# Kernel tuning notes

Hardware: AMD Instinct MI355X
Metric: run time of the kernel (lower is better)

Reference implementation:

```python
import jax, jax.numpy as jnp
import numpy as np

B, C, H, W = 2048, 6, 128, 96
OUT_H, OUT_W = 32, 24  # PIL resize((24, 32)) -> width=24, height=32

def setup_inputs() -> dict:
    key = jax.random.key(0)
    kx, ky = jax.random.split(key)
    x = jax.random.normal(kx, (B, C, H, W), dtype=jnp.float32)
    y = jax.random.randint(ky, (B,), 0, 10, dtype=jnp.int32)  # unused by forward
    return {"x": x, "y": y}

def reference(x, y):
    # Batched bilinear resize of every (batch, channel) image from (H, W) to (32, 24).
    # antialias=True matches PIL's BILINEAR triangle filter with scaled support
    # when downsampling. Batch/channel dims keep their size -> identity along them.
    resized = jax.image.resize(
        x, (x.shape[0], x.shape[1], OUT_H, OUT_W), method="bilinear", antialias=True
    ).astype(jnp.float32)
    # view(-1, 6, 768): each channel's 32*24 map flattens to a 768-dim feature.
    return resized.reshape(-1, 6, OUT_H * OUT_W)
```

## Files before the change

kernel.cpp:

```cpp
#include <hip/hip_runtime.h>


#define IMG_H 128
#define IMG_W 96
#define ROUT_H 32
#define ROUT_W 24
#define LDSTRIDE 100
#define MIDSTRIDE 25

__global__ __launch_bounds__(256, 2)
void resize_aa_kernel(const float* __restrict__ x, float* __restrict__ out) {
    __shared__ float s_in[IMG_H * LDSTRIDE];
    __shared__ float s_mid[IMG_H * MIDSTRIDE];

    const int img = blockIdx.x;
    const int tid = threadIdx.x;
    const float* __restrict__ src = x + (size_t)img * (IMG_H * IMG_W);

    const float4* __restrict__ src4 = (const float4*)src;
#pragma unroll
    for (int k = 0; k < 12; ++k) {
        int f = tid + k * 256;
        float4 g = src4[f];
        int row = f / 24;
        int c   = f - row * 24;
        *(float4*)(&s_in[row * LDSTRIDE + 4 * c]) = g;
    }
    __syncthreads();

    {
        int r = tid & 127;
        int h = tid >> 7;
        const float* rowp = &s_in[r * LDSTRIDE];
        int c0 = 12 * h;

        float4 prev = (h == 0) ? make_float4(0.f, 0.f, 0.f, 0.f)
                               : *(const float4*)(rowp + 4 * (c0 - 1));
        float4 cur  = *(const float4*)(rowp + 4 * c0);
#pragma unroll
        for (int j = 0; j < 12; ++j) {
            int ow = c0 + j;
            float4 next = (ow + 1 < ROUT_W) ? *(const float4*)(rowp + 4 * (ow + 1))
                                            : make_float4(0.f, 0.f, 0.f, 0.f);
            float w0 = 1.f/32, w1 = 3.f/32, w2 = 5.f/32, w3 = 7.f/32,
                  w4 = 7.f/32, w5 = 5.f/32, w6 = 3.f/32, w7 = 1.f/32;
            if (ow == 0) {
                const float s = 1.0f / 3.5f;
                w0 = 0.f;        w1 = 0.f;
                w2 = 0.625f * s; w3 = 0.875f * s; w4 = 0.875f * s;
                w5 = 0.625f * s; w6 = 0.375f * s; w7 = 0.125f * s;
            } else if (ow == ROUT_W - 1) {
                const float s = 1.0f / 3.5f;
                w0 = 0.125f * s; w1 = 0.375f * s; w2 = 0.625f * s;
                w3 = 0.875f * s; w4 = 0.875f * s; w5 = 0.625f * s;
                w6 = 0.f;        w7 = 0.f;
            }
            float acc = w0 * prev.z + w1 * prev.w
                      + w2 * cur.x  + w3 * cur.y + w4 * cur.z + w5 * cur.w
                      + w6 * next.x + w7 * next.y;
            s_mid[r * MIDSTRIDE + ow] = acc;
            prev = cur; cur = next;
        }
    }
    __syncthreads();

    float* __restrict__ dst = out + (size_t)img * (ROUT_H * ROUT_W);
#pragma unroll
    for (int k = 0; k < 3; ++k) {
        int idx = tid + k * 256;
        int oh = idx / ROUT_W;
        int ow = idx - oh * ROUT_W;
        int r0 = 4 * oh - 2;

        float w[8] = {1.f/32, 3.f/32, 5.f/32, 7.f/32, 7.f/32, 5.f/32, 3.f/32, 1.f/32};
        if (oh == 0) {
            const float s = 1.0f / 3.5f;
            w[0] = 0.f;        w[1] = 0.f;
            w[2] = 0.625f * s; w[3] = 0.875f * s; w[4] = 0.875f * s;
            w[5] = 0.625f * s; w[6] = 0.375f * s; w[7] = 0.125f * s;
        } else if (oh == ROUT_H - 1) {
            const float s = 1.0f / 3.5f;
            w[0] = 0.125f * s; w[1] = 0.375f * s; w[2] = 0.625f * s;
            w[3] = 0.875f * s; w[4] = 0.875f * s; w[5] = 0.625f * s;
            w[6] = 0.f;        w[7] = 0.f;
        }
        float acc = 0.f;
#pragma unroll
        for (int t = 0; t < 8; ++t) {
            int r = r0 + t;
            r = r < 0 ? 0 : (r > IMG_H - 1 ? IMG_H - 1 : r);
            acc += w[t] * s_mid[r * MIDSTRIDE + ow];
        }
        dst[idx] = acc;
    }
}

extern "C" void kernel_launch(void* const* d_in, const int* in_sizes, int n_in,
                              void* d_out, int out_size, void* d_ws, size_t ws_size,
                              hipStream_t stream) {
    const float* x = (const float*)d_in[0];
    float* out = (float*)d_out;
    const int n_img = 2048 * 6;
    resize_aa_kernel<<<n_img, 256, 0, stream>>>(x, out);
}
```

Baseline: 760.1 us.

## Filter vertically straight from global memory, drop input LDS staging

Reorders the separable resize so the vertical pass runs first, reading float4 columns directly from global memory into registers, and writes a small 32x96 intermediate to shared memory for the horizontal pass. This removes the full 128x96 shared-memory staging buffer and one barrier. It also lowers LDS use, which allows more blocks per CU (launch bound raised to 4). Each input row is now read from global memory by the two overlapping filter taps (stride 4, width 8), so global traffic roughly doubles in the L2/cache. The result depends on cache hits to absorb those repeated reads.

```diff
diff --git a/kernel.cpp b/kernel.cpp
--- a/kernel.cpp
+++ b/kernel.cpp
@@ -3,73 +3,23 @@
 
 #define IMG_H 128
 #define IMG_W 96
-#define ROUT_H 32
-#define ROUT_W 24
-#define LDSTRIDE 100
-#define MIDSTRIDE 25
+#define OH 32
+#define OW 24
+#define TSTR 100
 
-__global__ __launch_bounds__(256, 2)
+__global__ __launch_bounds__(256, 4)
 void resize_aa_kernel(const float* __restrict__ x, float* __restrict__ out) {
-    __shared__ float s_in[IMG_H * LDSTRIDE];
-    __shared__ float s_mid[IMG_H * MIDSTRIDE];
+    __shared__ float s_tmp[OH * TSTR];
 
     const int img = blockIdx.x;
     const int tid = threadIdx.x;
-    const float* __restrict__ src = x + (size_t)img * (IMG_H * IMG_W);
+    const float4* __restrict__ src4 = (const float4*)(x + (size_t)img * (IMG_H * IMG_W));
 
-    const float4* __restrict__ src4 = (const float4*)src;
-#pragma unroll
-    for (int k = 0; k < 12; ++k) {
-        int f = tid + k * 256;
-        float4 g = src4[f];
-        int row = f / 24;
-        int c   = f - row * 24;
-        *(float4*)(&s_in[row * LDSTRIDE + 4 * c]) = g;
-    }
-    __syncthreads();
-
-    {
-        int r = tid & 127;
-        int h = tid >> 7;
-        const float* rowp = &s_in[r * LDSTRIDE];
-        int c0 = 12 * h;
-
-        float4 prev = (h == 0) ? make_float4(0.f, 0.f, 0.f, 0.f)
-                               : *(const float4*)(rowp + 4 * (c0 - 1));
-        float4 cur  = *(const float4*)(rowp + 4 * c0);
-#pragma unroll
-        for (int j = 0; j < 12; ++j) {
-            int ow = c0 + j;
-            float4 next = (ow + 1 < ROUT_W) ? *(const float4*)(rowp + 4 * (ow + 1))
-                                            : make_float4(0.f, 0.f, 0.f, 0.f);
-            float w0 = 1.f/32, w1 = 3.f/32, w2 = 5.f/32, w3 = 7.f/32,
-                  w4 = 7.f/32, w5 = 5.f/32, w6 = 3.f/32, w7 = 1.f/32;
-            if (ow == 0) {
-                const float s = 1.0f / 3.5f;
-                w0 = 0.f;        w1 = 0.f;
-                w2 = 0.625f * s; w3 = 0.875f * s; w4 = 0.875f * s;
-                w5 = 0.625f * s; w6 = 0.375f * s; w7 = 0.125f * s;
-            } else if (ow == ROUT_W - 1) {
-                const float s = 1.0f / 3.5f;
-                w0 = 0.125f * s; w1 = 0.375f * s; w2 = 0.625f * s;
-                w3 = 0.875f * s; w4 = 0.875f * s; w5 = 0.625f * s;
-                w6 = 0.f;        w7 = 0.f;
-            }
-            float acc = w0 * prev.z + w1 * prev.w
-                      + w2 * cur.x  + w3 * cur.y + w4 * cur.z + w5 * cur.w
-                      + w6 * next.x + w7 * next.y;
-            s_mid[r * MIDSTRIDE + ow] = acc;
-            prev = cur; cur = next;
-        }
-    }
-    __syncthreads();
-
-    float* __restrict__ dst = out + (size_t)img * (ROUT_H * ROUT_W);
 #pragma unroll
     for (int k = 0; k < 3; ++k) {
         int idx = tid + k * 256;
-        int oh = idx / ROUT_W;
-        int ow = idx - oh * ROUT_W;
+        int oh = idx / OW;
+        int c  = idx - oh * OW;
         int r0 = 4 * oh - 2;
 
         float w[8] = {1.f/32, 3.f/32, 5.f/32, 7.f/32, 7.f/32, 5.f/32, 3.f/32, 1.f/32};
@@ -78,18 +28,59 @@
             w[0] = 0.f;        w[1] = 0.f;
             w[2] = 0.625f * s; w[3] = 0.875f * s; w[4] = 0.875f * s;
             w[5] = 0.625f * s; w[6] = 0.375f * s; w[7] = 0.125f * s;
-        } else if (oh == ROUT_H - 1) {
+        } else if (oh == OH - 1) {
             const float s = 1.0f / 3.5f;
             w[0] = 0.125f * s; w[1] = 0.375f * s; w[2] = 0.625f * s;
             w[3] = 0.875f * s; w[4] = 0.875f * s; w[5] = 0.625f * s;
             w[6] = 0.f;        w[7] = 0.f;
         }
-        float acc = 0.f;
+
+        float4 v[8];
 #pragma unroll
         for (int t = 0; t < 8; ++t) {
             int r = r0 + t;
             r = r < 0 ? 0 : (r > IMG_H - 1 ? IMG_H - 1 : r);
-            acc += w[t] * s_mid[r * MIDSTRIDE + ow];
+            v[t] = src4[r * (IMG_W / 4) + c];
+        }
+        float4 acc = make_float4(0.f, 0.f, 0.f, 0.f);
+#pragma unroll
+        for (int t = 0; t < 8; ++t) {
+            acc.x += w[t] * v[t].x;
+            acc.y += w[t] * v[t].y;
+            acc.z += w[t] * v[t].z;
+            acc.w += w[t] * v[t].w;
+        }
+        *(float4*)&s_tmp[oh * TSTR + 4 * c] = acc;
+    }
+    __syncthreads();
+
+    float* __restrict__ dst = out + (size_t)img * (OH * OW);
+#pragma unroll
+    for (int k = 0; k < 3; ++k) {
+        int idx = tid + k * 256;
+        int oh = idx / OW;
+        int ow = idx - oh * OW;
+        int c0 = 4 * ow - 2;
+
+        float w[8] = {1.f/32, 3.f/32, 5.f/32, 7.f/32, 7.f/32, 5.f/32, 3.f/32, 1.f/32};
+        if (ow == 0) {
+            const float s = 1.0f / 3.5f;
+            w[0] = 0.f;        w[1] = 0.f;
+            w[2] = 0.625f * s; w[3] = 0.875f * s; w[4] = 0.875f * s;
+            w[5] = 0.625f * s; w[6] = 0.375f * s; w[7] = 0.125f * s;
+        } else if (ow == OW - 1) {
+            const float s = 1.0f / 3.5f;
+            w[0] = 0.125f * s; w[1] = 0.375f * s; w[2] = 0.625f * s;
+            w[3] = 0.875f * s; w[4] = 0.875f * s; w[5] = 0.625f * s;
+            w[6] = 0.f;        w[7] = 0.f;
+        }
+
+        float acc = 0.f;
+#pragma unroll
+        for (int t = 0; t < 8; ++t) {
+            int cc = c0 + t;
+            cc = cc < 0 ? 0 : (cc > IMG_W - 1 ? IMG_W - 1 : cc);
+            acc += w[t] * s_tmp[oh * TSTR + cc];
         }
         dst[idx] = acc;
     }
```

Measured after the change: 764.2 us. No clear change (+0.5%).
